# Performance work log

Hardware: AMD Instinct MI355X
Metric: run time of the kernel (lower is better)

Reference implementation:

```python
import jax, jax.numpy as jnp
import numpy as np

N_NODES = 50000
N_EDGES = 1600000
IN_DIM = 128
HIDDEN = 256
N_CLASSES = 2
N_GRAPHS = 512
BN_EPS = 1e-5


def setup_inputs() -> dict:
    key = jax.random.key(0)
    ks = jax.random.split(key, 12)
    x = jax.random.normal(ks[0], (N_NODES, IN_DIM), dtype=jnp.float32)
    edge_index = jax.random.randint(ks[1], (2, N_EDGES), 0, N_NODES, dtype=jnp.int64)
    batch = jnp.sort(jax.random.randint(ks[2], (N_NODES,), 0, N_GRAPHS, dtype=jnp.int64))
    s1 = 1.0 / np.sqrt(IN_DIM)
    s2 = 1.0 / np.sqrt(HIDDEN)
    return {
        "x": x,
        "edge_index": edge_index,
        "batch": batch,
        # GIN MLP: Linear(in,hidden) -> BN -> ReLU -> Linear(hidden,hidden)
        "W1": jax.random.uniform(ks[3], (IN_DIM, HIDDEN), jnp.float32, -s1, s1),
        "b1": jnp.zeros((HIDDEN,), jnp.float32),
        "g1": jnp.ones((HIDDEN,), jnp.float32),
        "be1": jnp.zeros((HIDDEN,), jnp.float32),
        "W2": jax.random.uniform(ks[4], (HIDDEN, HIDDEN), jnp.float32, -s2, s2),
        "b2": jnp.zeros((HIDDEN,), jnp.float32),
        # attention gate: Linear(hidden, 1)
        "Wg": jax.random.uniform(ks[5], (HIDDEN, 1), jnp.float32, -s2, s2),
        "bg": jnp.zeros((1,), jnp.float32),
        # head: BN(hidden) -> Dropout(eval: identity) -> Linear(hidden, n_classes)
        "g2": jnp.ones((HIDDEN,), jnp.float32),
        "be2": jnp.zeros((HIDDEN,), jnp.float32),
        "Wh": jax.random.uniform(ks[6], (HIDDEN, N_CLASSES), jnp.float32, -s2, s2),
        "bh": jnp.zeros((N_CLASSES,), jnp.float32),
    }


def _batchnorm(h, gamma, beta):
    # training-mode BN: batch statistics over axis 0 (biased variance, as torch)
    mu = jnp.mean(h, axis=0)
    var = jnp.mean(jnp.square(h - mu), axis=0)
    return gamma * (h - mu) * jax.lax.rsqrt(var + BN_EPS) + beta


def reference(x, edge_index, batch, W1, b1, g1, be1, W2, b2, Wg, bg, g2, be2, Wh, bh):
    src, dst = edge_index[0], edge_index[1]
    # GINConv (eps=0): agg_i = sum_{j->i} x_j ; h = MLP(x + agg)
    agg = jax.ops.segment_sum(x[src], dst, num_segments=N_NODES)  # [N, in_dim]
    h = x + agg
    h = h @ W1 + b1                      # [N, hidden]
    h = jax.nn.relu(_batchnorm(h, g1, be1))
    h = h @ W2 + b2                      # [N, hidden]
    h = jax.nn.relu(h)                   # outer F.relu in forward
    # AttentionalAggregation: segment softmax of gate, weighted sum per graph
    gate = h @ Wg + bg                   # [N, 1]
    m = jax.ops.segment_max(gate, batch, num_segments=N_GRAPHS)  # [G, 1]
    e = jnp.exp(gate - m[batch])
    s = jax.ops.segment_sum(e, batch, num_segments=N_GRAPHS)     # [G, 1]
    alpha = e / s[batch]                 # [N, 1]
    pooled = jax.ops.segment_sum(alpha * h, batch, num_segments=N_GRAPHS)  # [G, hidden]
    # head: BN -> (Dropout eval = identity) -> Linear -> log_softmax
    z = _batchnorm(pooled, g2, be2) @ Wh + bh  # [G, n_classes]
    return jax.nn.log_softmax(z, axis=-1)
```

## Files before the change

kernel.cpp:

```cpp
#include <hip/hip_runtime.h>

typedef unsigned int u32;
typedef unsigned short ushort_t;
typedef __attribute__((ext_vector_type(8))) short bf16x8;
typedef __attribute__((ext_vector_type(4))) float f32x4;

#define PCAP 3072
#define OVFCAP 1600000

__device__ __forceinline__ float bf2f_lo(u32 u){
  union{u32 i; float f;} v; v.i = u<<16; return v.f;
}
__device__ __forceinline__ float bf2f_hi(u32 u){
  union{u32 i; float f;} v; v.i = u & 0xFFFF0000u; return v.f;
}
__device__ __forceinline__ u32 pack2bf(float a, float b){
  union{float f; u32 i;} va, vb; va.f=a; vb.f=b;
  u32 ra = (va.i + 0x7FFF + ((va.i>>16)&1)) >> 16;
  u32 rb = (vb.i + 0x7FFF + ((vb.i>>16)&1)) & 0xFFFF0000u;
  return ra | rb;
}
__device__ __forceinline__ ushort_t f2bf1(float f){
  union{float f; u32 i;} v; v.f=f;
  u32 r = v.i + 0x7FFF + ((v.i>>16)&1);
  return (ushort_t)(r>>16);
}

__global__ __launch_bounds__(256) void prep(const float* __restrict__ x, u32* __restrict__ xb, long nconv,
                                            const float* __restrict__ W1, ushort_t* __restrict__ W1t,
                                            const float* __restrict__ W2, ushort_t* __restrict__ W2t,
                                            int* __restrict__ bcursor, int* __restrict__ ovf_cnt, int NB){
  long blk = blockIdx.x;
  int tid = threadIdx.x;
  if(blk < nconv){
    long i = blk*256 + tid;
    float4 v = ((const float4*)x)[i];
    uint2 o; o.x = pack2bf(v.x, v.y); o.y = pack2bf(v.z, v.w);
    ((uint2*)xb)[i] = o;
  } else if(blk < nconv + 256){
    int n = (int)(blk - nconv);
    for(int k = tid; k < 128; k += 256) W1t[(size_t)n*128 + k] = f2bf1(W1[(size_t)k*256 + n]);
  } else if(blk < nconv + 512){
    int n = (int)(blk - nconv - 256);
    for(int k = tid; k < 256; k += 256) W2t[(size_t)n*256 + k] = f2bf1(W2[(size_t)k*256 + n]);
  } else {
    for(int i = tid; i < NB*16; i += 256) bcursor[i] = 0;
    if(tid == 0) *ovf_cnt = 0;
  }
}

__global__ __launch_bounds__(256) void binscatter_direct(const int* __restrict__ src, const int* __restrict__ dst,
                                                         int* __restrict__ bcursor, u32* __restrict__ pairs,
                                                         int* __restrict__ ovf, int* __restrict__ ovf_cnt,
                                                         int E, int N, int NB){
  __shared__ int hist[1024];
  __shared__ int base[1024];
  int e0 = blockIdx.x*4096;
  int e1 = min(e0+4096, E);
  for(int i=threadIdx.x; i<NB; i+=256) hist[i]=0;
  __syncthreads();
  for(int i=e0+threadIdx.x; i<e1; i+=256){
    int d = dst[i];
    if((u32)d >= (u32)N) d = 0;
    atomicAdd(&hist[d>>6], 1);
  }
  __syncthreads();
  for(int i=threadIdx.x; i<NB; i+=256){
    int c = hist[i];
    base[i] = c ? atomicAdd(&bcursor[i*16], c) : 0;
    hist[i] = 0;
  }
  __syncthreads();
  for(int i=e0+threadIdx.x; i<e1; i+=256){
    int d = dst[i]; if((u32)d >= (u32)N) d = 0;
    int s = src[i]; if((u32)s >= (u32)N) s = 0;
    int b = d>>6;
    int loc = atomicAdd(&hist[b], 1);
    int pos = base[b] + loc;
    if(pos < PCAP){
      pairs[(size_t)b*PCAP + pos] = (u32)s | (((u32)(d & 63))<<17);
    } else {
      int o = atomicAdd(ovf_cnt, 1);
      if(o < OVFCAP){ ovf[2*o] = s; ovf[2*o+1] = d; }
    }
  }
}

__global__ __launch_bounds__(512) void gather_bucket(const u32* __restrict__ xb,
                                                     const u32* __restrict__ pairs,
                                                     const int* __restrict__ bcursor,
                                                     const int* __restrict__ ovf, const int* __restrict__ ovf_cnt,
                                                     u32* __restrict__ h0b, int N){
  __shared__ int lsrc[PCAP];
  __shared__ int dcnt[64];
  __shared__ int dstart[65];
  __shared__ int dcur[64];
  __shared__ int s_ovfn;
  int b = blockIdx.x;
  int tid = threadIdx.x;
  int cnt = bcursor[b*16];
  if(cnt < 0) cnt = 0;
  int cl = min(cnt, PCAP);
  if(tid < 64) dcnt[tid] = 0;
  if(tid == 0){ int o = *ovf_cnt; s_ovfn = (o < 0) ? 0 : min(o, OVFCAP); }
  __syncthreads();
  const u32* mypairs = pairs + (size_t)b*PCAP;
  for(int i=tid; i<cl; i+=512){
    u32 u = mypairs[i];
    atomicAdd(&dcnt[(u>>17)&63], 1);
  }
  __syncthreads();
  if(tid==0){
    int run=0;
    #pragma unroll
    for(int j=0;j<64;j++){ dstart[j]=run; dcur[j]=run; run+=dcnt[j]; }
    dstart[64]=run;
  }
  __syncthreads();
  for(int i=tid; i<cl; i+=512){
    u32 u = mypairs[i];
    int pos = atomicAdd(&dcur[(u>>17)&63], 1);
    lsrc[pos] = (int)(u & 0x1FFFFu);
  }
  __syncthreads();
  int ovfn = s_ovfn;
  const uint4* xr = (const uint4*)xb;
  int slot = tid >> 4;
  int c = tid & 15;
  for(int pass=0; pass<2; pass++){
    int r = pass*32 + slot;
    int node = b*64 + r;
    if(node >= N) continue;
    uint4 xv = xr[(size_t)node*16 + c];
    float acc[8] = {
      bf2f_lo(xv.x), bf2f_hi(xv.x), bf2f_lo(xv.y), bf2f_hi(xv.y),
      bf2f_lo(xv.z), bf2f_hi(xv.z), bf2f_lo(xv.w), bf2f_hi(xv.w) };
    int ds = dstart[r], de = dstart[r+1];
    int j = ds;
    for(; j+8 <= de; j += 8){
      int s0=lsrc[j+0], s1=lsrc[j+1], s2=lsrc[j+2], s3=lsrc[j+3];
      int s4=lsrc[j+4], s5=lsrc[j+5], s6=lsrc[j+6], s7=lsrc[j+7];
      uint4 v0 = xr[(size_t)s0*16 + c];
      uint4 v1 = xr[(size_t)s1*16 + c];
      uint4 v2 = xr[(size_t)s2*16 + c];
      uint4 v3 = xr[(size_t)s3*16 + c];
      uint4 v4 = xr[(size_t)s4*16 + c];
      uint4 v5 = xr[(size_t)s5*16 + c];
      uint4 v6 = xr[(size_t)s6*16 + c];
      uint4 v7 = xr[(size_t)s7*16 + c];
      acc[0]+=bf2f_lo(v0.x)+bf2f_lo(v1.x)+bf2f_lo(v2.x)+bf2f_lo(v3.x)
             +bf2f_lo(v4.x)+bf2f_lo(v5.x)+bf2f_lo(v6.x)+bf2f_lo(v7.x);
      acc[1]+=bf2f_hi(v0.x)+bf2f_hi(v1.x)+bf2f_hi(v2.x)+bf2f_hi(v3.x)
             +bf2f_hi(v4.x)+bf2f_hi(v5.x)+bf2f_hi(v6.x)+bf2f_hi(v7.x);
      acc[2]+=bf2f_lo(v0.y)+bf2f_lo(v1.y)+bf2f_lo(v2.y)+bf2f_lo(v3.y)
             +bf2f_lo(v4.y)+bf2f_lo(v5.y)+bf2f_lo(v6.y)+bf2f_lo(v7.y);
      acc[3]+=bf2f_hi(v0.y)+bf2f_hi(v1.y)+bf2f_hi(v2.y)+bf2f_hi(v3.y)
             +bf2f_hi(v4.y)+bf2f_hi(v5.y)+bf2f_hi(v6.y)+bf2f_hi(v7.y);
      acc[4]+=bf2f_lo(v0.z)+bf2f_lo(v1.z)+bf2f_lo(v2.z)+bf2f_lo(v3.z)
             +bf2f_lo(v4.z)+bf2f_lo(v5.z)+bf2f_lo(v6.z)+bf2f_lo(v7.z);
      acc[5]+=bf2f_hi(v0.z)+bf2f_hi(v1.z)+bf2f_hi(v2.z)+bf2f_hi(v3.z)
             +bf2f_hi(v4.z)+bf2f_hi(v5.z)+bf2f_hi(v6.z)+bf2f_hi(v7.z);
      acc[6]+=bf2f_lo(v0.w)+bf2f_lo(v1.w)+bf2f_lo(v2.w)+bf2f_lo(v3.w)
             +bf2f_lo(v4.w)+bf2f_lo(v5.w)+bf2f_lo(v6.w)+bf2f_lo(v7.w);
      acc[7]+=bf2f_hi(v0.w)+bf2f_hi(v1.w)+bf2f_hi(v2.w)+bf2f_hi(v3.w)
             +bf2f_hi(v4.w)+bf2f_hi(v5.w)+bf2f_hi(v6.w)+bf2f_hi(v7.w);
    }
    for(; j < de; j++){
      int s = lsrc[j];
      uint4 v = xr[(size_t)s*16 + c];
      acc[0]+=bf2f_lo(v.x); acc[1]+=bf2f_hi(v.x);
      acc[2]+=bf2f_lo(v.y); acc[3]+=bf2f_hi(v.y);
      acc[4]+=bf2f_lo(v.z); acc[5]+=bf2f_hi(v.z);
      acc[6]+=bf2f_lo(v.w); acc[7]+=bf2f_hi(v.w);
    }
    if(ovfn > 0){
      for(int i=0;i<ovfn;i++){
        int s = ovf[2*i], d = ovf[2*i+1];
        if(d == node){
          if((u32)s >= (u32)N) s = 0;
          uint4 v = xr[(size_t)s*16 + c];
          acc[0]+=bf2f_lo(v.x); acc[1]+=bf2f_hi(v.x);
          acc[2]+=bf2f_lo(v.y); acc[3]+=bf2f_hi(v.y);
          acc[4]+=bf2f_lo(v.z); acc[5]+=bf2f_hi(v.z);
          acc[6]+=bf2f_lo(v.w); acc[7]+=bf2f_hi(v.w);
        }
      }
    }
    uint4 o;
    o.x = pack2bf(acc[0],acc[1]); o.y = pack2bf(acc[2],acc[3]);
    o.z = pack2bf(acc[4],acc[5]); o.w = pack2bf(acc[6],acc[7]);
    ((uint4*)h0b)[(size_t)node*16 + c] = o;
  }
}

template<int K, bool BNA, bool RELUOUT, bool GATE, bool ABF16, bool OUTBF16, bool STATS>
__global__ __launch_bounds__(512) void gemm_mfma(const void* __restrict__ Ap, const ushort_t* __restrict__ Wt,
                                                 const float* __restrict__ bias,
                                                 const float* __restrict__ scale, const float* __restrict__ shift,
                                                 void* __restrict__ Cp, int M,
                                                 const float* __restrict__ Wg, const float* __restrict__ bg,
                                                 float* __restrict__ gate,
                                                 float* __restrict__ psum, float* __restrict__ pq, int NS){
  __shared__ uint4 Al[8*129];
  __shared__ uint4 Bl[8*257];
  __shared__ float gacc[128];
  __shared__ float sstat[512];
  const int tid  = threadIdx.x;
  const int lane = tid & 63;
  const int wave = tid >> 6;
  const int lm   = lane & 15;
  const int q    = lane >> 4;
  const int mhalf= wave >> 2;
  const int nq   = wave & 3;
  const int m0   = blockIdx.x * 128;

  if(GATE && tid < 128) gacc[tid] = 0.f;
  if(STATS){ sstat[tid] = 0.f; }

  f32x4 acc[4][4];
  #pragma unroll
  for(int i=0;i<4;i++)
    #pragma unroll
    for(int j=0;j<4;j++) acc[i][j] = (f32x4){0.f,0.f,0.f,0.f};

  for(int k0=0; k0<K; k0+=64){
    #pragma unroll
    for(int i=0;i<2;i++){
      int idx = tid*2 + i;
      int m = idx >> 3, c = idx & 7;
      int grow = m0 + m;
      int kk = k0 + c*8;
      uint4 v = make_uint4(0,0,0,0);
      if(ABF16){
        if(grow < M) v = *(const uint4*)((const ushort_t*)Ap + (size_t)grow*K + kk);
        if(BNA){
          float f0=bf2f_lo(v.x), f1=bf2f_hi(v.x), f2=bf2f_lo(v.y), f3=bf2f_hi(v.y);
          float f4=bf2f_lo(v.z), f5=bf2f_hi(v.z), f6=bf2f_lo(v.w), f7=bf2f_hi(v.w);
          float4 s0 = *(const float4*)(scale+kk),  s1 = *(const float4*)(scale+kk+4);
          float4 t0 = *(const float4*)(shift+kk),  t1 = *(const float4*)(shift+kk+4);
          f0=fmaxf(fmaf(s0.x,f0,t0.x),0.f); f1=fmaxf(fmaf(s0.y,f1,t0.y),0.f);
          f2=fmaxf(fmaf(s0.z,f2,t0.z),0.f); f3=fmaxf(fmaf(s0.w,f3,t0.w),0.f);
          f4=fmaxf(fmaf(s1.x,f4,t1.x),0.f); f5=fmaxf(fmaf(s1.y,f5,t1.y),0.f);
          f6=fmaxf(fmaf(s1.z,f6,t1.z),0.f); f7=fmaxf(fmaf(s1.w,f7,t1.w),0.f);
          v.x = pack2bf(f0,f1); v.y = pack2bf(f2,f3);
          v.z = pack2bf(f4,f5); v.w = pack2bf(f6,f7);
        }
      } else {
        float4 u0 = make_float4(0,0,0,0), u1 = make_float4(0,0,0,0);
        if(grow < M){
          u0 = *(const float4*)((const float*)Ap + (size_t)grow*K + kk);
          u1 = *(const float4*)((const float*)Ap + (size_t)grow*K + kk + 4);
        }
        if(BNA){
          float4 s0 = *(const float4*)(scale+kk),  s1 = *(const float4*)(scale+kk+4);
          float4 t0 = *(const float4*)(shift+kk),  t1 = *(const float4*)(shift+kk+4);
          u0.x=fmaxf(fmaf(s0.x,u0.x,t0.x),0.f); u0.y=fmaxf(fmaf(s0.y,u0.y,t0.y),0.f);
          u0.z=fmaxf(fmaf(s0.z,u0.z,t0.z),0.f); u0.w=fmaxf(fmaf(s0.w,u0.w,t0.w),0.f);
          u1.x=fmaxf(fmaf(s1.x,u1.x,t1.x),0.f); u1.y=fmaxf(fmaf(s1.y,u1.y,t1.y),0.f);
          u1.z=fmaxf(fmaf(s1.z,u1.z,t1.z),0.f); u1.w=fmaxf(fmaf(s1.w,u1.w,t1.w),0.f);
        }
        v.x = pack2bf(u0.x,u0.y); v.y = pack2bf(u0.z,u0.w);
        v.z = pack2bf(u1.x,u1.y); v.w = pack2bf(u1.z,u1.w);
      }
      Al[c*129 + m] = v;
    }
    #pragma unroll
    for(int i=0;i<4;i++){
      int idx = tid*4 + i;
      int n = idx >> 3, c = idx & 7;
      Bl[c*257 + n] = *(const uint4*)(Wt + (size_t)n*K + k0 + c*8);
    }
    __syncthreads();
    #pragma unroll
    for(int ks=0; ks<2; ks++){
      int cc = ks*4 + q;
      bf16x8 af[4], bfr[4];
      #pragma unroll
      for(int mi=0; mi<4; mi++)
        af[mi] = *((const bf16x8*)&Al[cc*129 + mhalf*64 + mi*16 + lm]);
      #pragma unroll
      for(int ni=0; ni<4; ni++)
        bfr[ni] = *((const bf16x8*)&Bl[cc*257 + nq*64 + ni*16 + lm]);
      #pragma unroll
      for(int mi=0; mi<4; mi++)
        #pragma unroll
        for(int ni=0; ni<4; ni++)
          acc[mi][ni] = __builtin_amdgcn_mfma_f32_16x16x32_bf16(af[mi], bfr[ni], acc[mi][ni], 0, 0, 0);
    }
    __syncthreads();
  }

  float bb[4], wgv[4];
  float cs[4] = {0.f,0.f,0.f,0.f};
  float cq[4] = {0.f,0.f,0.f,0.f};
  #pragma unroll
  for(int ni=0; ni<4; ni++){
    int col = nq*64 + ni*16 + lm;
    bb[ni] = bias[col];
    if(GATE) wgv[ni] = Wg[col];
  }
  #pragma unroll
  for(int mi=0; mi<4; mi++){
    int rowloc0 = mhalf*64 + mi*16 + q*4;
    float gp[4] = {0.f,0.f,0.f,0.f};
    #pragma unroll
    for(int ni=0; ni<4; ni++){
      int col = nq*64 + ni*16 + lm;
      f32x4 o = acc[mi][ni];
      #pragma unroll
      for(int r=0; r<4; r++){
        float v = o[r] + bb[ni];
        if(RELUOUT) v = fmaxf(v, 0.f);
        int row = m0 + rowloc0 + r;
        if(row < M){
          if(OUTBF16) ((ushort_t*)Cp)[(size_t)row*256 + col] = f2bf1(v);
          else        ((float*)Cp)[(size_t)row*256 + col] = v;
          if(STATS){ cs[ni] += v; cq[ni] = fmaf(v, v, cq[ni]); }
        }
        if(GATE) gp[r] = fmaf(v, wgv[ni], gp[r]);
      }
    }
    if(GATE){
      #pragma unroll
      for(int r=0; r<4; r++){
        if(m0 + rowloc0 + r < M) atomicAdd(&gacc[rowloc0 + r], gp[r]);
      }
    }
  }
  if(STATS){
    __syncthreads();
    #pragma unroll
    for(int ni=0; ni<4; ni++){
      int col = nq*64 + ni*16 + lm;
      atomicAdd(&sstat[col], cs[ni]);
      atomicAdd(&sstat[256+col], cq[ni]);
    }
    __syncthreads();
    if(tid < 256){
      psum[(size_t)tid*NS + blockIdx.x] = sstat[tid];
      pq[(size_t)tid*NS + blockIdx.x]   = sstat[256+tid];
    }
  }
  if(GATE){
    __syncthreads();
    if(tid < 128){
      int row = m0 + tid;
      if(row < M) gate[row] = gacc[tid] + bg[0];
    }
  }
}

__global__ __launch_bounds__(256) void col_stats2(const float* __restrict__ h, float* __restrict__ psum,
                                                  float* __restrict__ pq, int M, int rpb, int nblk){
  int b = blockIdx.x;
  int g = threadIdx.x >> 6;
  int lane = threadIdx.x & 63;
  int c0 = lane*4;
  int r0 = b*rpb;
  int r1 = min(r0+rpb, M);
  float4 s4 = make_float4(0.f,0.f,0.f,0.f);
  float4 q4 = make_float4(0.f,0.f,0.f,0.f);
  for(int r=r0+g; r<r1; r+=4){
    float4 v = *(const float4*)(h + (size_t)r*256 + c0);
    s4.x+=v.x; s4.y+=v.y; s4.z+=v.z; s4.w+=v.w;
    q4.x=fmaf(v.x,v.x,q4.x); q4.y=fmaf(v.y,v.y,q4.y);
    q4.z=fmaf(v.z,v.z,q4.z); q4.w=fmaf(v.w,v.w,q4.w);
  }
  __shared__ float ls[1024];
  __shared__ float lq[1024];
  *(float4*)&ls[g*256+c0] = s4;
  *(float4*)&lq[g*256+c0] = q4;
  __syncthreads();
  if(threadIdx.x < 64){
    #pragma unroll
    for(int j=0;j<4;j++){
      int c = c0+j;
      float s = ls[c]+ls[256+c]+ls[512+c]+ls[768+c];
      float q = lq[c]+lq[256+c]+lq[512+c]+lq[768+c];
      psum[(size_t)c*nblk + b] = s;
      pq[(size_t)c*nblk + b]   = q;
    }
  }
}

__global__ __launch_bounds__(512) void stats_fin(const float* __restrict__ psum, const float* __restrict__ pq,
                                                 const float* __restrict__ gamma, const float* __restrict__ beta,
                                                 float* __restrict__ scale, float* __restrict__ shift,
                                                 int nblk, int NS, float invM){
  __shared__ float red[512];
  int t = threadIdx.x;
  const float* src = (t<256) ? (psum + (size_t)t*NS) : (pq + (size_t)(t-256)*NS);
  float s = 0.f;
  int i = 0;
  for(; i+4 <= nblk; i += 4){
    float4 v = *(const float4*)(src+i);
    s += v.x+v.y+v.z+v.w;
  }
  for(; i < nblk; i++) s += src[i];
  red[t]=s; __syncthreads();
  if(t<256){
    float mu  = red[t]*invM;
    float var = fmaxf(red[256+t]*invM - mu*mu, 0.f);
    float sc  = gamma[t] * rsqrtf(var + 1e-5f);
    scale[t]=sc; shift[t]=fmaf(-mu, sc, beta[t]);
  }
}

__global__ __launch_bounds__(512) void pool_k(const ushort_t* __restrict__ h2b, const float* __restrict__ gate,
                                              const int* __restrict__ batch, float* __restrict__ pooled, int N){
  int g = blockIdx.x;
  __shared__ int sb[2];
  __shared__ float red[8];
  __shared__ float s_m, s_inv;
  __shared__ float la[256];
  __shared__ float sa[8*256];
  int t = threadIdx.x;
  if(t < 2){
    int target = g + t;
    int lo=0, hi=N;
    while(lo<hi){ int mid=(lo+hi)>>1; if(batch[mid] < target) lo=mid+1; else hi=mid; }
    sb[t] = lo;
  }
  __syncthreads();
  int beg = sb[0], end = sb[1];
  float mx = -1e30f;
  for(int i=beg+t; i<end; i+=512) mx = fmaxf(mx, gate[i]);
  #pragma unroll
  for(int d=32; d>0; d>>=1) mx = fmaxf(mx, __shfl_down(mx, d, 64));
  if((t&63)==0) red[t>>6] = mx;
  __syncthreads();
  if(t==0){
    float m = red[0];
    #pragma unroll
    for(int w=1; w<8; w++) m = fmaxf(m, red[w]);
    s_m = m;
  }
  __syncthreads();
  float m = s_m;
  float s = 0.f;
  for(int i=beg+t; i<end; i+=512) s += expf(gate[i]-m);
  #pragma unroll
  for(int d=32; d>0; d>>=1) s += __shfl_down(s, d, 64);
  if((t&63)==0) red[t>>6] = s;
  __syncthreads();
  if(t==0){
    float tot = 0.f;
    #pragma unroll
    for(int w=0; w<8; w++) tot += red[w];
    s_inv = (tot > 0.f) ? 1.f/tot : 0.f;
  }
  __syncthreads();
  float inv = s_inv;
  const uint2* h2w2 = (const uint2*)h2b;
  int cp = t & 63;
  int rowgrp = t >> 6;
  float a0=0.f, a1=0.f, a2=0.f, a3=0.f;
  for(int ci=beg; ci<end; ci+=256){
    int chunk = min(256, end-ci);
    if(t < 256) la[t] = (t < chunk) ? expf(gate[ci+t]-m)*inv : 0.f;
    __syncthreads();
    for(int j=rowgrp; j<chunk; j+=8){
      uint2 h = h2w2[(size_t)(ci+j)*64 + cp];
      float w = la[j];
      a0 = fmaf(w, bf2f_lo(h.x), a0);
      a1 = fmaf(w, bf2f_hi(h.x), a1);
      a2 = fmaf(w, bf2f_lo(h.y), a2);
      a3 = fmaf(w, bf2f_hi(h.y), a3);
    }
    __syncthreads();
  }
  *(float4*)&sa[rowgrp*256 + cp*4] = make_float4(a0,a1,a2,a3);
  __syncthreads();
  if(t < 256){
    float r = sa[t] + sa[256+t] + sa[512+t] + sa[768+t]
            + sa[1024+t] + sa[1280+t] + sa[1536+t] + sa[1792+t];
    pooled[g*256 + t] = r;
  }
}

__global__ __launch_bounds__(256) void head_k(const float* __restrict__ pooled,
                                              const float* __restrict__ sc2, const float* __restrict__ sh2,
                                              const float* __restrict__ Wh, const float* __restrict__ bh,
                                              float* __restrict__ out, int G){
  int w = (blockIdx.x*256 + threadIdx.x) >> 6;
  int l = threadIdx.x & 63;
  if(w >= G) return;
  float4 v  = *(const float4*)(pooled + (size_t)w*256 + l*4);
  float4 sc = *(const float4*)(sc2 + l*4);
  float4 sh = *(const float4*)(sh2 + l*4);
  float vv[4] = { fmaf(sc.x,v.x,sh.x), fmaf(sc.y,v.y,sh.y), fmaf(sc.z,v.z,sh.z), fmaf(sc.w,v.w,sh.w) };
  float4 w0 = *(const float4*)(Wh + (size_t)l*8);
  float4 w1 = *(const float4*)(Wh + (size_t)l*8 + 4);
  float a0 = vv[0]*w0.x + vv[1]*w0.z + vv[2]*w1.x + vv[3]*w1.z;
  float a1 = vv[0]*w0.y + vv[1]*w0.w + vv[2]*w1.y + vv[3]*w1.w;
  #pragma unroll
  for(int d=32; d>0; d>>=1){ a0 += __shfl_down(a0,d,64); a1 += __shfl_down(a1,d,64); }
  if(l==0){
    float z0 = a0 + bh[0];
    float z1 = a1 + bh[1];
    float mz = fmaxf(z0,z1);
    float lse = mz + logf(expf(z0-mz) + expf(z1-mz));
    out[w*2]   = z0 - lse;
    out[w*2+1] = z1 - lse;
  }
}

extern "C" void kernel_launch(void* const* d_in, const int* in_sizes, int n_in,
                              void* d_out, int out_size, void* d_ws, size_t ws_size,
                              hipStream_t stream){
  const float* x   = (const float*)d_in[0];
  const int*   ei  = (const int*)d_in[1];
  const int*   bat = (const int*)d_in[2];
  const float* W1  = (const float*)d_in[3];
  const float* b1  = (const float*)d_in[4];
  const float* g1  = (const float*)d_in[5];
  const float* be1 = (const float*)d_in[6];
  const float* W2  = (const float*)d_in[7];
  const float* b2  = (const float*)d_in[8];
  const float* Wg  = (const float*)d_in[9];
  const float* bg  = (const float*)d_in[10];
  const float* g2  = (const float*)d_in[11];
  const float* be2 = (const float*)d_in[12];
  const float* Wh  = (const float*)d_in[13];
  const float* bh  = (const float*)d_in[14];

  const int N = in_sizes[0] / 128;
  const int E = in_sizes[1] / 2;
  const int G = out_size / 2;
  const int NB = (N + 63) >> 6;
  const int gblocks = (N + 127)/128;
  const int NS1 = (gblocks + 7) & ~7;
  const int NBLK2 = 64;

  char* ws = (char*)d_ws;
  u32*   h0b    = (u32*)ws;
  u32*   xb     = (u32*)(ws + 12800000);
  u32*   pairs  = (u32*)(ws + 25600000);
  int*   bcursor= (int*)(ws + 35210240);
  int*   ovf_cnt= (int*)(ws + 35275776);
  int*   ovf    = (int*)(ws + 35276032);
  ushort_t* h2b = (ushort_t*)ws;
  u32*   h1b    = (u32*)(ws + 51200000);
  char*  p2 = ws + 102400000;
  float* psum1 = (float*)p2;          p2 += 256*NS1*4;
  float* pq1   = (float*)p2;          p2 += 256*NS1*4;
  float* psum2 = (float*)p2;          p2 += 256*NBLK2*4;
  float* pq2   = (float*)p2;          p2 += 256*NBLK2*4;
  float* sc1   = (float*)p2;          p2 += 1024;
  float* sh1   = (float*)p2;          p2 += 1024;
  float* sc2   = (float*)p2;          p2 += 1024;
  float* sh2   = (float*)p2;          p2 += 1024;
  float* gate  = (float*)p2;          p2 += (size_t)N*4 + 4096;
  float* pooled= (float*)p2;          p2 += (size_t)G*256*4;
  ushort_t* W1t = (ushort_t*)p2;      p2 += 256*128*2;
  ushort_t* W2t = (ushort_t*)p2;      p2 += 256*256*2;

  const int* src = ei;
  const int* dst = ei + E;

  long nconv = (long)N*128/4/256;
  prep<<<(int)(nconv + 512 + 1), 256, 0, stream>>>(x, xb, nconv, W1, W1t, W2, W2t, bcursor, ovf_cnt, NB);

  int nchunk = (E + 4095)/4096;
  binscatter_direct<<<nchunk, 256, 0, stream>>>(src, dst, bcursor, pairs, ovf, ovf_cnt, E, N, NB);
  gather_bucket<<<NB, 512, 0, stream>>>(xb, pairs, bcursor, ovf, ovf_cnt, h0b, N);

  gemm_mfma<128,false,false,false,true,true,true><<<gblocks, 512, 0, stream>>>(
      h0b, W1t, b1, nullptr, nullptr, h1b, N, nullptr, nullptr, nullptr, psum1, pq1, NS1);
  stats_fin<<<1, 512, 0, stream>>>(psum1, pq1, g1, be1, sc1, sh1, gblocks, NS1, 1.0f/(float)N);
  gemm_mfma<256,true,true,true,true,true,false><<<gblocks, 512, 0, stream>>>(
      h1b, W2t, b2, sc1, sh1, h2b, N, Wg, bg, gate, nullptr, nullptr, 0);

  pool_k<<<G, 512, 0, stream>>>(h2b, gate, bat, pooled, N);
  int rpb2 = (G + NBLK2 - 1)/NBLK2;
  col_stats2<<<NBLK2, 256, 0, stream>>>(pooled, psum2, pq2, G, rpb2, NBLK2);
  stats_fin<<<1, 512, 0, stream>>>(psum2, pq2, g2, be2, sc2, sh2, NBLK2, NBLK2, 1.0f/(float)G);
  head_k<<<(G+3)/4, 256, 0, stream>>>(pooled, sc2, sh2, Wh, bh, (float*)d_out, G);
}
```

Before: 341.7 us.

## Fuse pooled BN stats, finalize and head into one last-block kernel; shuffle-reduce gate

Replaces the three tail kernels (col_stats2, stats_fin, head_k) with a single tail_k kernel. Each block writes partial column sums, and the last block to finish, detected through an atomic counter that prep resets, computes the BN scale and shift and runs the head for all graphs. This removes two kernel launches. Separately, the gate partial sums in the second GEMM are reduced with wave shuffles before the LDS atomic, which cuts shared-memory atomic traffic. The trade is that the whole head now runs serially in one block of 4 waves, and the code depends on the counter being reset at the start of every call.

After: 404.5 us. 1.18x slower.

```diff
diff --git a/kernel.cpp b/kernel.cpp
--- a/kernel.cpp
+++ b/kernel.cpp
@@ -45,7 +45,7 @@
     for(int k = tid; k < 256; k += 256) W2t[(size_t)n*256 + k] = f2bf1(W2[(size_t)k*256 + n]);
   } else {
     for(int i = tid; i < NB*16; i += 256) bcursor[i] = 0;
-    if(tid == 0) *ovf_cnt = 0;
+    if(tid == 0){ ovf_cnt[0] = 0; ovf_cnt[16] = 0; }
   }
 }
 
@@ -323,7 +323,10 @@
     if(GATE){
       #pragma unroll
       for(int r=0; r<4; r++){
-        if(m0 + rowloc0 + r < M) atomicAdd(&gacc[rowloc0 + r], gp[r]);
+        float gv = gp[r];
+        #pragma unroll
+        for(int d=1; d<16; d<<=1) gv += __shfl_xor(gv, d, 64);
+        if(lm == 0 && m0 + rowloc0 + r < M) atomicAdd(&gacc[rowloc0 + r], gv);
       }
     }
   }
@@ -346,39 +349,6 @@
     if(tid < 128){
       int row = m0 + tid;
       if(row < M) gate[row] = gacc[tid] + bg[0];
-    }
-  }
-}
-
-__global__ __launch_bounds__(256) void col_stats2(const float* __restrict__ h, float* __restrict__ psum,
-                                                  float* __restrict__ pq, int M, int rpb, int nblk){
-  int b = blockIdx.x;
-  int g = threadIdx.x >> 6;
-  int lane = threadIdx.x & 63;
-  int c0 = lane*4;
-  int r0 = b*rpb;
-  int r1 = min(r0+rpb, M);
-  float4 s4 = make_float4(0.f,0.f,0.f,0.f);
-  float4 q4 = make_float4(0.f,0.f,0.f,0.f);
-  for(int r=r0+g; r<r1; r+=4){
-    float4 v = *(const float4*)(h + (size_t)r*256 + c0);
-    s4.x+=v.x; s4.y+=v.y; s4.z+=v.z; s4.w+=v.w;
-    q4.x=fmaf(v.x,v.x,q4.x); q4.y=fmaf(v.y,v.y,q4.y);
-    q4.z=fmaf(v.z,v.z,q4.z); q4.w=fmaf(v.w,v.w,q4.w);
-  }
-  __shared__ float ls[1024];
-  __shared__ float lq[1024];
-  *(float4*)&ls[g*256+c0] = s4;
-  *(float4*)&lq[g*256+c0] = q4;
-  __syncthreads();
-  if(threadIdx.x < 64){
-    #pragma unroll
-    for(int j=0;j<4;j++){
-      int c = c0+j;
-      float s = ls[c]+ls[256+c]+ls[512+c]+ls[768+c];
-      float q = lq[c]+lq[256+c]+lq[512+c]+lq[768+c];
-      psum[(size_t)c*nblk + b] = s;
-      pq[(size_t)c*nblk + b]   = q;
     }
   }
 }
@@ -478,30 +448,84 @@
   }
 }
 
-__global__ __launch_bounds__(256) void head_k(const float* __restrict__ pooled,
-                                              const float* __restrict__ sc2, const float* __restrict__ sh2,
+__global__ __launch_bounds__(256) void tail_k(const float* __restrict__ pooled,
+                                              const float* __restrict__ g2, const float* __restrict__ be2,
                                               const float* __restrict__ Wh, const float* __restrict__ bh,
-                                              float* __restrict__ out, int G){
-  int w = (blockIdx.x*256 + threadIdx.x) >> 6;
-  int l = threadIdx.x & 63;
-  if(w >= G) return;
-  float4 v  = *(const float4*)(pooled + (size_t)w*256 + l*4);
-  float4 sc = *(const float4*)(sc2 + l*4);
-  float4 sh = *(const float4*)(sh2 + l*4);
-  float vv[4] = { fmaf(sc.x,v.x,sh.x), fmaf(sc.y,v.y,sh.y), fmaf(sc.z,v.z,sh.z), fmaf(sc.w,v.w,sh.w) };
-  float4 w0 = *(const float4*)(Wh + (size_t)l*8);
-  float4 w1 = *(const float4*)(Wh + (size_t)l*8 + 4);
-  float a0 = vv[0]*w0.x + vv[1]*w0.z + vv[2]*w1.x + vv[3]*w1.z;
-  float a1 = vv[0]*w0.y + vv[1]*w0.w + vv[2]*w1.y + vv[3]*w1.w;
-  #pragma unroll
-  for(int d=32; d>0; d>>=1){ a0 += __shfl_down(a0,d,64); a1 += __shfl_down(a1,d,64); }
-  if(l==0){
-    float z0 = a0 + bh[0];
-    float z1 = a1 + bh[1];
-    float mz = fmaxf(z0,z1);
-    float lse = mz + logf(expf(z0-mz) + expf(z1-mz));
-    out[w*2]   = z0 - lse;
-    out[w*2+1] = z1 - lse;
+                                              float* __restrict__ psum2, float* __restrict__ pq2,
+                                              int* __restrict__ done, float* __restrict__ out, int G){
+  int b = blockIdx.x;
+  int t = threadIdx.x;
+  __shared__ float ls[1024];
+  __shared__ float lq[1024];
+  __shared__ int s_old;
+  {
+    int grp = t >> 6, lane = t & 63, c0 = lane*4;
+    int r0 = b*8, r1 = min(r0+8, G);
+    float4 s4 = make_float4(0.f,0.f,0.f,0.f);
+    float4 q4 = make_float4(0.f,0.f,0.f,0.f);
+    for(int r=r0+grp; r<r1; r+=4){
+      float4 v = *(const float4*)(pooled + (size_t)r*256 + c0);
+      s4.x+=v.x; s4.y+=v.y; s4.z+=v.z; s4.w+=v.w;
+      q4.x=fmaf(v.x,v.x,q4.x); q4.y=fmaf(v.y,v.y,q4.y);
+      q4.z=fmaf(v.z,v.z,q4.z); q4.w=fmaf(v.w,v.w,q4.w);
+    }
+    *(float4*)&ls[grp*256+c0] = s4;
+    *(float4*)&lq[grp*256+c0] = q4;
+    __syncthreads();
+    if(t < 64){
+      #pragma unroll
+      for(int j=0;j<4;j++){
+        int c = c0+j;
+        float s = ls[c]+ls[256+c]+ls[512+c]+ls[768+c];
+        float q = lq[c]+lq[256+c]+lq[512+c]+lq[768+c];
+        psum2[(size_t)c*64 + b] = s;
+        pq2[(size_t)c*64 + b]   = q;
+      }
+    }
+  }
+  __threadfence();
+  if(t==0) s_old = atomicAdd(done, 1);
+  __syncthreads();
+  if(s_old != 63) return;
+  __threadfence();
+  __shared__ float ssc[256], ssh[256];
+  {
+    int c = t;
+    const float* srcs = psum2 + (size_t)c*64;
+    const float* srcq = pq2 + (size_t)c*64;
+    float s=0.f, q=0.f;
+    for(int i=0;i<64;i+=4){
+      float4 v = *(const float4*)(srcs+i); s += v.x+v.y+v.z+v.w;
+      float4 w = *(const float4*)(srcq+i); q += w.x+w.y+w.z+w.w;
+    }
+    float invG = 1.f/(float)G;
+    float mu = s*invG;
+    float var = fmaxf(q*invG - mu*mu, 0.f);
+    float sc = g2[c]*rsqrtf(var + 1e-5f);
+    ssc[c] = sc; ssh[c] = fmaf(-mu, sc, be2[c]);
+  }
+  __syncthreads();
+  int wv = t >> 6, l = t & 63;
+  for(int w=wv; w<G; w+=4){
+    float4 v  = *(const float4*)(pooled + (size_t)w*256 + l*4);
+    float vv0 = fmaf(ssc[l*4+0], v.x, ssh[l*4+0]);
+    float vv1 = fmaf(ssc[l*4+1], v.y, ssh[l*4+1]);
+    float vv2 = fmaf(ssc[l*4+2], v.z, ssh[l*4+2]);
+    float vv3 = fmaf(ssc[l*4+3], v.w, ssh[l*4+3]);
+    float4 w0 = *(const float4*)(Wh + (size_t)l*8);
+    float4 w1 = *(const float4*)(Wh + (size_t)l*8 + 4);
+    float a0 = vv0*w0.x + vv1*w0.z + vv2*w1.x + vv3*w1.z;
+    float a1 = vv0*w0.y + vv1*w0.w + vv2*w1.y + vv3*w1.w;
+    #pragma unroll
+    for(int d=32; d>0; d>>=1){ a0 += __shfl_down(a0,d,64); a1 += __shfl_down(a1,d,64); }
+    if(l==0){
+      float z0 = a0 + bh[0];
+      float z1 = a1 + bh[1];
+      float mz = fmaxf(z0,z1);
+      float lse = mz + logf(expf(z0-mz) + expf(z1-mz));
+      out[w*2]   = z0 - lse;
+      out[w*2+1] = z1 - lse;
+    }
   }
 }
 
@@ -530,7 +554,6 @@
   const int NB = (N + 63) >> 6;
   const int gblocks = (N + 127)/128;
   const int NS1 = (gblocks + 7) & ~7;
-  const int NBLK2 = 64;
 
   char* ws = (char*)d_ws;
   u32*   h0b    = (u32*)ws;
@@ -544,12 +567,10 @@
   char*  p2 = ws + 102400000;
   float* psum1 = (float*)p2;          p2 += 256*NS1*4;
   float* pq1   = (float*)p2;          p2 += 256*NS1*4;
-  float* psum2 = (float*)p2;          p2 += 256*NBLK2*4;
-  float* pq2   = (float*)p2;          p2 += 256*NBLK2*4;
+  float* psum2 = (float*)p2;          p2 += 256*64*4;
+  float* pq2   = (float*)p2;          p2 += 256*64*4;
   float* sc1   = (float*)p2;          p2 += 1024;
   float* sh1   = (float*)p2;          p2 += 1024;
-  float* sc2   = (float*)p2;          p2 += 1024;
-  float* sh2   = (float*)p2;          p2 += 1024;
   float* gate  = (float*)p2;          p2 += (size_t)N*4 + 4096;
   float* pooled= (float*)p2;          p2 += (size_t)G*256*4;
   ushort_t* W1t = (ushort_t*)p2;      p2 += 256*128*2;
@@ -572,8 +593,5 @@
       h1b, W2t, b2, sc1, sh1, h2b, N, Wg, bg, gate, nullptr, nullptr, 0);
 
   pool_k<<<G, 512, 0, stream>>>(h2b, gate, bat, pooled, N);
-  int rpb2 = (G + NBLK2 - 1)/NBLK2;
-  col_stats2<<<NBLK2, 256, 0, stream>>>(pooled, psum2, pq2, G, rpb2, NBLK2);
-  stats_fin<<<1, 512, 0, stream>>>(psum2, pq2, g2, be2, sc2, sh2, NBLK2, NBLK2, 1.0f/(float)G);
-  head_k<<<(G+3)/4, 256, 0, stream>>>(pooled, sc2, sh2, Wh, bh, (float*)d_out, G);
-}
+  tail_k<<<64, 256, 0, stream>>>(pooled, g2, be2, Wh, bh, psum2, pq2, &ovf_cnt[16], (float*)d_out, G);
+}
```
